# Kernel tuning notes

Hardware: AMD Instinct MI355X
Metric: run time of the kernel (lower is better)

## Reference

```python
import jax, jax.numpy as jnp
import numpy as np

B, D, S, F, C, H, OUT = 4, 60, 512, 158, 64, 128, 1
LN_EPS = 1e-5


def setup_inputs() -> dict:
    key = jax.random.key(0)
    ks = jax.random.split(key, 12)
    g = lambda k, shape, s=0.05: jax.random.normal(k, shape, dtype=jnp.float32) * s
    return dict(
        x=jax.random.normal(ks[0], (B, D, S, F), dtype=jnp.float32),
        feature_mask=jax.random.randint(ks[1], (B, D, S), 0, 2).astype(bool),
        wq=g(ks[2], (F, C)), bq=jnp.zeros((C,), jnp.float32),
        wk=g(ks[3], (F, C)), bk=jnp.zeros((C,), jnp.float32),
        wv=g(ks[4], (F, C)), bv=jnp.zeros((C,), jnp.float32),
        ln_g=jnp.ones((F + C,), jnp.float32), ln_b=jnp.zeros((F + C,), jnp.float32),
        w_ih=g(ks[5], (3 * H, F + C)), w_hh=g(ks[6], (3 * H, H)),
        b_ih=jnp.zeros((3 * H,), jnp.float32), b_hh=jnp.zeros((3 * H,), jnp.float32),
        w1=g(ks[7], (H, H // 2)), b1=jnp.zeros((H // 2,), jnp.float32),
        w2=g(ks[8], (H // 2, OUT)), b2=jnp.zeros((OUT,), jnp.float32),
    )


def reference(x, feature_mask, wq, bq, wk, bk, wv, bv, ln_g, ln_b,
              w_ih, w_hh, b_ih, b_hh, w1, b1, w2, b2):
    b, d, s, f = x.shape
    c = wq.shape[1]
    h_dim = w_hh.shape[1]

    # --- market context attention, vectorized over (batch, days) ---
    Q = x @ wq + bq            # (B,D,S,C)
    K = x @ wk + bk
    V = x @ wv + bv
    scores = jnp.einsum('bdsc,bdtc->bdst', Q, K) / jnp.sqrt(jnp.float32(c))
    scores = jnp.where(feature_mask[:, :, None, :], scores, -1e9)  # mask keys
    attn = jax.nn.softmax(scores, axis=-1)
    ctx = jnp.einsum('bdst,bdtc->bdsc', attn, V)       # (B,D,S,C)
    ctx = jnp.where(feature_mask[..., None], ctx, 0.0)  # mask queries
    denom = jnp.maximum(feature_mask.sum(axis=2), 1).astype(x.dtype)  # (B,D)
    market = ctx.sum(axis=2) / denom[..., None]         # (B,D,C)

    # --- concat + layernorm ---
    aug = jnp.concatenate(
        [x, jnp.broadcast_to(market[:, :, None, :], (b, d, s, c))], axis=-1)
    mu = aug.mean(-1, keepdims=True)
    var = aug.var(-1, keepdims=True)
    aug = (aug - mu) / jnp.sqrt(var + LN_EPS) * ln_g + ln_b  # (B,D,S,F+C)

    # --- GRU over days, batch = B*S independent sequences ---
    seq = aug.transpose(1, 0, 2, 3).reshape(d, b * s, f + c)  # (D, N, F+C)
    x_proj = seq @ w_ih.T + b_ih                               # (D, N, 3H)

    def step(h, xp):
        hp = h @ w_hh.T + b_hh
        xr, xz, xn = jnp.split(xp, 3, axis=-1)
        hr, hz, hn = jnp.split(hp, 3, axis=-1)
        r = jax.nn.sigmoid(xr + hr)
        z = jax.nn.sigmoid(xz + hz)
        n = jnp.tanh(xn + r * hn)
        return (1.0 - z) * n + z * h, None

    h0 = jnp.zeros((b * s, h_dim), x.dtype)
    h_last, _ = jax.lax.scan(step, h0, x_proj)  # last-step output
    h_last = h_last.reshape(b, s, h_dim)

    # --- output head (dropout inactive in eval) ---
    hid = jax.nn.relu(h_last @ w1 + b1)
    return hid @ w2 + b2  # (B, S, OUT)
```

## Files before the change

kernel.cpp:

```cpp
#include <hip/hip_runtime.h>
#include <hip/hip_bf16.h>
#include <math.h>

#define BB 4
#define DD 60
#define SS 512
#define FF 158
#define CC 64
#define HH 128
#define FC 222
#define G3 384
#define NN 2048
#define BDN 240

#define L2E  1.44269504f
#define L2E2 2.88539008f
#define QSCALE 0.18033688f

typedef _Float16 f16x8 __attribute__((ext_vector_type(8)));
typedef float f32x4 __attribute__((ext_vector_type(4)));

__device__ __forceinline__ float exp2_hw(float x){ return __builtin_amdgcn_exp2f(x); }
__device__ __forceinline__ float rcp_hw(float x){ return __builtin_amdgcn_rcpf(x); }

__global__ void prep_kernel(const float* __restrict__ w_ih,
                            const float* __restrict__ wq, const float* __restrict__ wk,
                            const float* __restrict__ w_hh,
                            _Float16* __restrict__ wf16, _Float16* __restrict__ wqk,
                            _Float16* __restrict__ whh16){
    int idx = blockIdx.x*256 + threadIdx.x;
    if (idx < 384*224){
        int n = idx / 224, k = idx % 224;
        float sc = (n < 256) ? L2E : L2E2;
        wf16[idx] = (k < FC) ? (_Float16)(w_ih[n*FC + k] * sc) : (_Float16)0.0f;
    } else if (idx < 384*224 + 128*160){
        int i2 = idx - 384*224;
        int n = i2 / 160, k = i2 % 160;
        float v = 0.0f;
        if (k < FF)
            v = (n < 64) ? wq[k*CC + n] : wk[k*CC + (n-64)];
        wqk[i2] = (_Float16)v;
    } else {
        int i3 = idx - (384*224 + 128*160);
        if (i3 < 384*128){
            int n = i3 / 128;
            float sc = (n < 256) ? L2E : L2E2;
            whh16[i3] = (_Float16)(w_hh[i3] * sc);
        }
    }
}

__global__ __launch_bounds__(256) void qk_kernel(const float* __restrict__ x,
                           const _Float16* __restrict__ wqk,
                           const float* __restrict__ bq, const float* __restrict__ bk,
                           _Float16* __restrict__ Qh, _Float16* __restrict__ Kh){
    __shared__ _Float16 xa[5][64][40];
    int tid  = threadIdx.x;
    int lane = tid & 63, wv = tid >> 6;
    int col  = lane & 15, quad = lane >> 4;
    int row0 = blockIdx.x * 64;

    f16x8 bfr[2][5];
    #pragma unroll
    for (int nt = 0; nt < 2; ++nt){
        int n = wv*32 + nt*16 + col;
        #pragma unroll
        for (int kq = 0; kq < 5; ++kq)
            bfr[nt][kq] = *(const f16x8*)&wqk[n*160 + kq*32 + quad*8];
    }

    if (tid < 128){
        int r = tid >> 1;
        xa[4][r][30 + (tid & 1)] = (_Float16)0.0f;
    }
    {
        const float4* xb4 = (const float4*)(x + (size_t)row0*FF);
        #pragma unroll
        for (int j = 0; j < 10; ++j){
            int i = tid + j*256;
            if (i < 2528){
                float4 v = xb4[i];
                int base = i*4;
                #pragma unroll
                for (int e = 0; e < 4; ++e){
                    int idx = base + e;
                    int r = idx / 158;
                    int k = idx - r*158;
                    xa[k >> 5][r][k & 31] = (_Float16)((&v.x)[e]);
                }
            }
        }
    }
    __syncthreads();

    float bias[2];
    #pragma unroll
    for (int nt = 0; nt < 2; ++nt){
        int n = wv*32 + nt*16 + col;
        bias[nt] = (n < 64) ? bq[n] : bk[n-64];
    }

    #pragma unroll 1
    for (int mt = 0; mt < 4; ++mt){
        f16x8 a[5];
        #pragma unroll
        for (int kq = 0; kq < 5; ++kq)
            a[kq] = *(const f16x8*)&xa[kq][mt*16 + col][quad*8];
        #pragma unroll
        for (int nt = 0; nt < 2; ++nt){
            f32x4 c = {0.0f, 0.0f, 0.0f, 0.0f};
            #pragma unroll
            for (int kq = 0; kq < 5; ++kq)
                c = __builtin_amdgcn_mfma_f32_16x16x32_f16(a[kq], bfr[nt][kq], c, 0, 0, 0);
            int n = wv*32 + nt*16 + col;
            #pragma unroll
            for (int reg = 0; reg < 4; ++reg){
                int row = row0 + mt*16 + quad*4 + reg;
                float val = c[reg] + bias[nt];
                if (n < 64) Qh[(size_t)row*CC + n]      = (_Float16)(val * QSCALE);
                else        Kh[(size_t)row*CC + (n-64)] = (_Float16)val;
            }
        }
    }
}

__global__ __launch_bounds__(512) void attn_kernel(const _Float16* __restrict__ Qh,
                                                   const _Float16* __restrict__ Kh,
                                                   const int* __restrict__ mask,
                                                   const float* __restrict__ x,
                                                   const float* __restrict__ wv,
                                                   const float* __restrict__ bv,
                                                   float* __restrict__ market){
    __shared__ _Float16 kf[2][512][32];
    __shared__ float w_sh[512];
    __shared__ float mk_lds[512];

    int tid  = threadIdx.x;
    int bd   = blockIdx.x;
    int lane = tid & 63, wvw = tid >> 6;
    int col  = lane & 15, quad = lane >> 4;

    const _Float16* qb = Qh + (size_t)(bd*SS)*CC;
    const _Float16* kb = Kh + (size_t)(bd*SS)*CC;

    {
        int t = tid;
        w_sh[t] = 0.0f;
        mk_lds[t] = (mask[bd*SS + t] != 0) ? 1.0f : 0.0f;
    }
    for (int i = tid; i < 4096; i += 512){
        int t = i >> 3, ch = i & 7;
        *(f16x8*)&kf[ch >> 2][t][(ch & 3)*8] = *(const f16x8*)&kb[t*CC + ch*8];
    }

    f16x8 a0[4], a1[4];
    #pragma unroll
    for (int af = 0; af < 4; ++af){
        int row = wvw*64 + af*16 + col;
        a0[af] = *(const f16x8*)&qb[row*CC + quad*8];
        a1[af] = *(const f16x8*)&qb[row*CC + 32 + quad*8];
    }
    __syncthreads();

    float lacc[4][4] = {{0,0,0,0},{0,0,0,0},{0,0,0,0},{0,0,0,0}};
    #pragma unroll 2
    for (int kt = 0; kt < 32; ++kt){
        f16x8 b0 = *(const f16x8*)&kf[0][kt*16 + col][quad*8];
        f16x8 b1 = *(const f16x8*)&kf[1][kt*16 + col][quad*8];
        float mkv = mk_lds[kt*16 + col];
        #pragma unroll
        for (int af = 0; af < 4; ++af){
            f32x4 c = {0.0f, 0.0f, 0.0f, 0.0f};
            c = __builtin_amdgcn_mfma_f32_16x16x32_f16(a0[af], b0, c, 0, 0, 0);
            c = __builtin_amdgcn_mfma_f32_16x16x32_f16(a1[af], b1, c, 0, 0, 0);
            #pragma unroll
            for (int reg = 0; reg < 4; ++reg)
                lacc[af][reg] += exp2_hw(c[reg]) * mkv;
        }
    }
    float crv[4][4];
    #pragma unroll
    for (int af = 0; af < 4; ++af){
        #pragma unroll
        for (int reg = 0; reg < 4; ++reg){
            float l = lacc[af][reg];
            l += __shfl_xor(l, 1, 64);
            l += __shfl_xor(l, 2, 64);
            l += __shfl_xor(l, 4, 64);
            l += __shfl_xor(l, 8, 64);
            int row = wvw*64 + af*16 + quad*4 + reg;
            crv[af][reg] = mk_lds[row] * rcp_hw(l);
        }
    }

    #pragma unroll 2
    for (int kt = 0; kt < 32; ++kt){
        f16x8 b0 = *(const f16x8*)&kf[0][kt*16 + col][quad*8];
        f16x8 b1 = *(const f16x8*)&kf[1][kt*16 + col][quad*8];
        float s = 0.0f;
        #pragma unroll
        for (int af = 0; af < 4; ++af){
            f32x4 c = {0.0f, 0.0f, 0.0f, 0.0f};
            c = __builtin_amdgcn_mfma_f32_16x16x32_f16(a0[af], b0, c, 0, 0, 0);
            c = __builtin_amdgcn_mfma_f32_16x16x32_f16(a1[af], b1, c, 0, 0, 0);
            #pragma unroll
            for (int reg = 0; reg < 4; ++reg)
                s = fmaf(exp2_hw(c[reg]), crv[af][reg], s);
        }
        s += __shfl_xor(s, 16, 64);
        s += __shfl_xor(s, 32, 64);
        if (quad == 0)
            atomicAdd(&w_sh[kt*16 + col], s);
    }
    __syncthreads();

    w_sh[tid] *= mk_lds[tid];
    __syncthreads();

    float* part = (float*)kf;
    {
        int tg = tid >> 8;
        int kk = tid & 255;
        float acc = 0.0f;
        if (kk < FF){
            const float* xb = x + ((size_t)bd*SS + tg*256)*FF + kk;
            #pragma unroll 8
            for (int t = 0; t < 256; ++t)
                acc = fmaf(w_sh[tg*256 + t], xb[(size_t)t*FF], acc);
        }
        part[tg*256 + kk] = acc;
    }
    __syncthreads();
    if (tid < 64){
        int c = tid;
        float m = 0.0f;
        for (int k = 0; k < FF; ++k){
            float y = part[k] + part[256 + k];
            m = fmaf(y, wv[k*CC + c], m);
        }
        float cnt = 0.0f, sw = 0.0f;
        #pragma unroll
        for (int j = 0; j < 8; ++j){
            cnt += mk_lds[c + 64*j];
            sw  += w_sh[c + 64*j];
        }
        #pragma unroll
        for (int o = 1; o < 64; o <<= 1){
            cnt += __shfl_xor(cnt, o, 64);
            sw  += __shfl_xor(sw,  o, 64);
        }
        market[bd*CC + c] = (m + sw*bv[c]) * rcp_hw(fmaxf(cnt, 1.0f));
    }
}

__global__ __launch_bounds__(512, 2) void xproj_kernel(const float* __restrict__ x,
                             const float* __restrict__ market,
                             const float* __restrict__ ln_g, const float* __restrict__ ln_b,
                             const _Float16* __restrict__ wf16, const float* __restrict__ b_ih,
                             _Float16* __restrict__ XP){
    __shared__ _Float16 aug[7][64][32];
    int tid  = threadIdx.x;
    int lane = tid & 63, wv = tid >> 6;
    int col  = lane & 15, quad = lane >> 4;
    int row0 = blockIdx.x * 64;

    f16x8 bfr[3][7];
    #pragma unroll
    for (int nt = 0; nt < 3; ++nt){
        int n = wv*48 + nt*16 + col;
        #pragma unroll
        for (int kq = 0; kq < 7; ++kq)
            bfr[nt][kq] = *(const f16x8*)&wf16[n*224 + kq*32 + quad*8];
    }

    {
        int wrow = wv*8 + (lane >> 3);
        int g    = lane & 7;
        int row  = row0 + wrow;
        int d = row / NN, n = row % NN;
        int b = n >> 9, s = n & 511;
        const float* xr = &x[((size_t)((b*DD + d)*SS) + s)*FF];
        const float* mr = &market[(b*DD + d)*CC];
        float v[28];
        float sum = 0.0f, sq = 0.0f;
        #pragma unroll
        for (int j = 0; j < 28; ++j){
            int f = g + 8*j;
            float vv = 0.0f;
            if (f < FF) vv = xr[f];
            else if (f < FC) vv = mr[f - FF];
            v[j] = vv;
            sum += vv; sq += vv*vv;
        }
        sum += __shfl_xor(sum,1,64); sq += __shfl_xor(sq,1,64);
        sum += __shfl_xor(sum,2,64); sq += __shfl_xor(sq,2,64);
        sum += __shfl_xor(sum,4,64); sq += __shfl_xor(sq,4,64);
        float mu   = sum * (1.0f/222.0f);
        float var  = sq * (1.0f/222.0f) - mu*mu;
        float rstd = rsqrtf(var + 1e-5f);
        #pragma unroll
        for (int j = 0; j < 28; ++j){
            int f = g + 8*j;
            float val = (f < FC) ? ((v[j]-mu)*rstd*ln_g[f] + ln_b[f]) : 0.0f;
            aug[f>>5][wrow][f&31] = (_Float16)val;
        }
    }
    __syncthreads();

    float bias[3];
    #pragma unroll
    for (int nt = 0; nt < 3; ++nt){
        int n = wv*48 + nt*16 + col;
        bias[nt] = b_ih[n] * ((n < 256) ? L2E : L2E2);
    }
    #pragma unroll 1
    for (int mt = 0; mt < 4; ++mt){
        f16x8 a[7];
        #pragma unroll
        for (int kq = 0; kq < 7; ++kq)
            a[kq] = *(const f16x8*)&aug[kq][mt*16 + col][quad*8];
        #pragma unroll
        for (int nt = 0; nt < 3; ++nt){
            f32x4 c = {0.0f, 0.0f, 0.0f, 0.0f};
            #pragma unroll
            for (int kq = 0; kq < 7; ++kq)
                c = __builtin_amdgcn_mfma_f32_16x16x32_f16(a[kq], bfr[nt][kq], c, 0, 0, 0);
            int nn = wv*48 + nt*16 + col;
            #pragma unroll
            for (int reg = 0; reg < 4; ++reg){
                int m = quad*4 + reg;
                XP[(size_t)(row0 + mt*16 + m)*G3 + nn] = (_Float16)(c[reg] + bias[nt]);
            }
        }
    }
}

#define XLOAD(dst, base_) do{                                                   \
    _Pragma("unroll") for (int hf_ = 0; hf_ < 2; ++hf_)                         \
    _Pragma("unroll") for (int rg_ = 0; rg_ < 4; ++rg_)                         \
    _Pragma("unroll") for (int g_ = 0; g_ < 3; ++g_)                            \
        dst[hf_][rg_][g_] = (base_)[rg_*G3 + g_*HH + hf_*16];                   \
}while(0)

#define BARRIER_NODRAIN() asm volatile("s_waitcnt lgkmcnt(0)\ns_barrier" ::: "memory")

#define GRU_STEP(PRD, PWR, XC, XPF, DOPF) do{                                   \
    if (DOPF) { XLOAD(XPF, xp_d + 2*DSTR); }                                    \
    f16x8 a_[4];                                                                \
    _Pragma("unroll") for (int kq = 0; kq < 4; ++kq)                            \
        a_[kq] = *(const f16x8*)&hfrag[PRD][kq][col][quad*8];                   \
    f32x4 c_[3][2];                                                             \
    _Pragma("unroll") for (int g = 0; g < 3; ++g)                               \
    _Pragma("unroll") for (int hf = 0; hf < 2; ++hf){                           \
        f32x4 acc = {0.0f, 0.0f, 0.0f, 0.0f};                                   \
        _Pragma("unroll") for (int kq = 0; kq < 4; ++kq)                        \
            acc = __builtin_amdgcn_mfma_f32_16x16x32_f16(a_[kq], bfr[g][hf][kq], acc, 0,0,0); \
        c_[g][hf] = acc;                                                        \
    }                                                                           \
    _Pragma("unroll") for (int hf = 0; hf < 2; ++hf)                            \
    _Pragma("unroll") for (int rg = 0; rg < 4; ++rg){                           \
        float r_ = rcp_hw(1.0f + exp2_hw(-((float)XC[hf][rg][0] + c_[0][hf][rg] + bh[0][hf]))); \
        float z_ = rcp_hw(1.0f + exp2_hw(-((float)XC[hf][rg][1] + c_[1][hf][rg] + bh[1][hf]))); \
        float e_ = exp2_hw((float)XC[hf][rg][2] + r_*(c_[2][hf][rg] + bh[2][hf])); \
        float n_ = 1.0f - 2.0f*rcp_hw(e_ + 1.0f);                               \
        float h_ = n_ + z_*(hcur[hf][rg] - n_);                                 \
        hcur[hf][rg] = h_;                                                      \
        hfrag[PWR][w][quad*4 + rg][hf*16 + col] = (_Float16)h_;                 \
    }                                                                           \
    xp_d += DSTR;                                                               \
    BARRIER_NODRAIN();                                                          \
}while(0)

__global__ __launch_bounds__(256, 1) void gru_kernel(const _Float16* __restrict__ XP,
                                                     const _Float16* __restrict__ whh16,
                                                     const float* __restrict__ b_hh,
                                                     const float* __restrict__ w1, const float* __restrict__ b1,
                                                     const float* __restrict__ w2, const float* __restrict__ b2,
                                                     float* __restrict__ out){
    __shared__ _Float16 hfrag[2][4][16][40];
    __shared__ float h_sh[16][132];

    const int tid  = threadIdx.x;
    const int lane = tid & 63, w = tid >> 6;
    const int col  = lane & 15, quad = lane >> 4;
    const int row0 = blockIdx.x * 16;

    for (int i = tid; i < 2*4*16*40; i += 256)
        ((_Float16*)hfrag)[i] = (_Float16)0.0f;

    f16x8 bfr[3][2][4];
    #pragma unroll
    for (int g = 0; g < 3; ++g)
    #pragma unroll
    for (int hf = 0; hf < 2; ++hf){
        int n = g*HH + w*32 + hf*16 + col;
        #pragma unroll
        for (int kq = 0; kq < 4; ++kq)
            bfr[g][hf][kq] = *(const f16x8*)&whh16[(size_t)n*HH + kq*32 + quad*8];
    }

    float bh[3][2];
    #pragma unroll
    for (int g = 0; g < 3; ++g)
    #pragma unroll
    for (int hf = 0; hf < 2; ++hf)
        bh[g][hf] = b_hh[g*HH + w*32 + hf*16 + col] * ((g < 2) ? L2E : L2E2);

    const size_t DSTR = (size_t)NN * G3;
    const _Float16* xp_d = XP + (size_t)(row0 + quad*4)*G3 + (w*32 + col);

    _Float16 xA[2][4][3], xB[2][4][3], xC[2][4][3];
    XLOAD(xA, xp_d);
    XLOAD(xB, xp_d + DSTR);

    float hcur[2][4] = {{0,0,0,0},{0,0,0,0}};
    __syncthreads();

    #pragma unroll 1
    for (int ch = 0; ch < 10; ++ch){
        const int pf = (ch < 9);
        GRU_STEP(0, 1, xA, xC, 1);
        GRU_STEP(1, 0, xB, xA, 1);
        GRU_STEP(0, 1, xC, xB, 1);
        GRU_STEP(1, 0, xA, xC, 1);
        GRU_STEP(0, 1, xB, xA, pf);
        GRU_STEP(1, 0, xC, xB, pf);
    }

    #pragma unroll
    for (int hf = 0; hf < 2; ++hf)
    #pragma unroll
    for (int rg = 0; rg < 4; ++rg)
        h_sh[quad*4 + rg][w*32 + hf*16 + col] = hcur[hf][rg];
    __syncthreads();

    {
        int c2 = tid & 63;
        int rb = tid >> 6;
        #pragma unroll
        for (int rr = 0; rr < 4; ++rr){
            int r = rb*4 + rr;
            float acc = 0.0f;
            #pragma unroll 8
            for (int k = 0; k < 128; ++k)
                acc = fmaf(h_sh[r][k], w1[k*64 + c2], acc);
            float hid = fmaxf(acc + b1[c2], 0.0f);
            float o = hid * w2[c2];
            #pragma unroll
            for (int off = 1; off < 64; off <<= 1) o += __shfl_xor(o, off, 64);
            if (c2 == 0) out[row0 + r] = o + b2[0];
        }
    }
}

extern "C" void kernel_launch(void* const* d_in, const int* in_sizes, int n_in,
                              void* d_out, int out_size, void* d_ws, size_t ws_size,
                              hipStream_t stream) {
    const float* x    = (const float*)d_in[0];
    const int*   mask = (const int*)d_in[1];
    const float* wq   = (const float*)d_in[2];
    const float* bq   = (const float*)d_in[3];
    const float* wk   = (const float*)d_in[4];
    const float* bk   = (const float*)d_in[5];
    const float* wv   = (const float*)d_in[6];
    const float* bv   = (const float*)d_in[7];
    const float* ln_g = (const float*)d_in[8];
    const float* ln_b = (const float*)d_in[9];
    const float* w_ih = (const float*)d_in[10];
    const float* w_hh = (const float*)d_in[11];
    const float* b_ih = (const float*)d_in[12];
    const float* b_hh = (const float*)d_in[13];
    const float* w1   = (const float*)d_in[14];
    const float* b1   = (const float*)d_in[15];
    const float* w2   = (const float*)d_in[16];
    const float* b2   = (const float*)d_in[17];

    float* ws = (float*)d_ws;
    _Float16* Qh  = (_Float16*)ws;
    _Float16* Kh  = (_Float16*)(ws + 3932160);
    _Float16* XP  = (_Float16*)ws;
    float* market = ws + 23592960;
    _Float16* wf16 = (_Float16*)(ws + 23608320);
    _Float16* wqk  = (_Float16*)(ws + 23651328);
    _Float16* whh16= (_Float16*)(ws + 23666688);

    prep_kernel<<<648, 256, 0, stream>>>(w_ih, wq, wk, w_hh, wf16, wqk, whh16);
    qk_kernel<<<1920, 256, 0, stream>>>(x, wqk, bq, bk, Qh, Kh);
    attn_kernel<<<240, 512, 0, stream>>>(Qh, Kh, mask, x, wv, bv, market);
    xproj_kernel<<<1920, 512, 0, stream>>>(x, market, ln_g, ln_b, wf16, b_ih, XP);
    gru_kernel<<<128, 256, 0, stream>>>(XP, whh16, b_hh, w1, b1, w2, b2, (float*)d_out);
}
```

Measured before the change: 346.8 us.

## Store GRU input projections in MFMA-fragment layout for vectorized loads

The xproj kernel now writes XP in a packed per-16-row-block layout where each gate column holds 4 consecutive row values contiguously. Each thread then issues one 8-byte store instead of four scattered 2-byte stores. The GRU kernel reads its per-step inputs with six f16x4 loads instead of 24 scalar half loads, which shortens the load path on the serial recurrence. The risk is less coalesced write patterns in xproj and more complex indexing.

```diff
diff --git a/kernel.cpp b/kernel.cpp
--- a/kernel.cpp
+++ b/kernel.cpp
@@ -18,6 +18,7 @@
 #define QSCALE 0.18033688f
 
 typedef _Float16 f16x8 __attribute__((ext_vector_type(8)));
+typedef _Float16 f16x4 __attribute__((ext_vector_type(4)));
 typedef float f32x4 __attribute__((ext_vector_type(4)));
 
 __device__ __forceinline__ float exp2_hw(float x){ return __builtin_amdgcn_exp2f(x); }
@@ -257,7 +258,7 @@
                              const float* __restrict__ market,
                              const float* __restrict__ ln_g, const float* __restrict__ ln_b,
                              const _Float16* __restrict__ wf16, const float* __restrict__ b_ih,
-                             _Float16* __restrict__ XP){
+                             _Float16* __restrict__ XPP){
     __shared__ _Float16 aug[7][64][32];
     int tid  = threadIdx.x;
     int lane = tid & 63, wv = tid >> 6;
@@ -313,12 +314,15 @@
         int n = wv*48 + nt*16 + col;
         bias[nt] = b_ih[n] * ((n < 256) ? L2E : L2E2);
     }
+    const int d    = row0 / NN;
+    const int blk0 = (row0 % NN) >> 4;
     #pragma unroll 1
     for (int mt = 0; mt < 4; ++mt){
         f16x8 a[7];
         #pragma unroll
         for (int kq = 0; kq < 7; ++kq)
             a[kq] = *(const f16x8*)&aug[kq][mt*16 + col][quad*8];
+        _Float16* obase = XPP + ((size_t)(d*128 + blk0 + mt)*G3) * 16 + quad*4;
         #pragma unroll
         for (int nt = 0; nt < 3; ++nt){
             f32x4 c = {0.0f, 0.0f, 0.0f, 0.0f};
@@ -326,20 +330,23 @@
             for (int kq = 0; kq < 7; ++kq)
                 c = __builtin_amdgcn_mfma_f32_16x16x32_f16(a[kq], bfr[nt][kq], c, 0, 0, 0);
             int nn = wv*48 + nt*16 + col;
-            #pragma unroll
-            for (int reg = 0; reg < 4; ++reg){
-                int m = quad*4 + reg;
-                XP[(size_t)(row0 + mt*16 + m)*G3 + nn] = (_Float16)(c[reg] + bias[nt]);
-            }
+            f16x4 pk;
+            pk[0] = (_Float16)(c[0] + bias[nt]);
+            pk[1] = (_Float16)(c[1] + bias[nt]);
+            pk[2] = (_Float16)(c[2] + bias[nt]);
+            pk[3] = (_Float16)(c[3] + bias[nt]);
+            *(f16x4*)(obase + (size_t)nn*16) = pk;
         }
     }
 }
 
 #define XLOAD(dst, base_) do{                                                   \
-    _Pragma("unroll") for (int hf_ = 0; hf_ < 2; ++hf_)                         \
-    _Pragma("unroll") for (int rg_ = 0; rg_ < 4; ++rg_)                         \
-    _Pragma("unroll") for (int g_ = 0; g_ < 3; ++g_)                            \
-        dst[hf_][rg_][g_] = (base_)[rg_*G3 + g_*HH + hf_*16];                   \
+    dst[0][0] = *(const f16x4*)((base_));                                       \
+    dst[0][1] = *(const f16x4*)((base_) + 128*16);                              \
+    dst[0][2] = *(const f16x4*)((base_) + 256*16);                              \
+    dst[1][0] = *(const f16x4*)((base_) + 16*16);                               \
+    dst[1][1] = *(const f16x4*)((base_) + 144*16);                              \
+    dst[1][2] = *(const f16x4*)((base_) + 272*16);                              \
 }while(0)
 
 #define BARRIER_NODRAIN() asm volatile("s_waitcnt lgkmcnt(0)\ns_barrier" ::: "memory")
@@ -359,9 +366,9 @@
     }                                                                           \
     _Pragma("unroll") for (int hf = 0; hf < 2; ++hf)                            \
     _Pragma("unroll") for (int rg = 0; rg < 4; ++rg){                           \
-        float r_ = rcp_hw(1.0f + exp2_hw(-((float)XC[hf][rg][0] + c_[0][hf][rg] + bh[0][hf]))); \
-        float z_ = rcp_hw(1.0f + exp2_hw(-((float)XC[hf][rg][1] + c_[1][hf][rg] + bh[1][hf]))); \
-        float e_ = exp2_hw((float)XC[hf][rg][2] + r_*(c_[2][hf][rg] + bh[2][hf])); \
+        float r_ = rcp_hw(1.0f + exp2_hw(-((float)XC[hf][0][rg] + c_[0][hf][rg] + bh[0][hf]))); \
+        float z_ = rcp_hw(1.0f + exp2_hw(-((float)XC[hf][1][rg] + c_[1][hf][rg] + bh[1][hf]))); \
+        float e_ = exp2_hw((float)XC[hf][2][rg] + r_*(c_[2][hf][rg] + bh[2][hf])); \
         float n_ = 1.0f - 2.0f*rcp_hw(e_ + 1.0f);                               \
         float h_ = n_ + z_*(hcur[hf][rg] - n_);                                 \
         hcur[hf][rg] = h_;                                                      \
@@ -371,7 +378,7 @@
     BARRIER_NODRAIN();                                                          \
 }while(0)
 
-__global__ __launch_bounds__(256, 1) void gru_kernel(const _Float16* __restrict__ XP,
+__global__ __launch_bounds__(256, 1) void gru_kernel(const _Float16* __restrict__ XPP,
                                                      const _Float16* __restrict__ whh16,
                                                      const float* __restrict__ b_hh,
                                                      const float* __restrict__ w1, const float* __restrict__ b1,
@@ -406,10 +413,10 @@
     for (int hf = 0; hf < 2; ++hf)
         bh[g][hf] = b_hh[g*HH + w*32 + hf*16 + col] * ((g < 2) ? L2E : L2E2);
 
-    const size_t DSTR = (size_t)NN * G3;
-    const _Float16* xp_d = XP + (size_t)(row0 + quad*4)*G3 + (w*32 + col);
-
-    _Float16 xA[2][4][3], xB[2][4][3], xC[2][4][3];
+    const size_t DSTR = (size_t)128 * G3 * 16;
+    const _Float16* xp_d = XPP + ((size_t)blockIdx.x*G3 + (w*32 + col))*16 + quad*4;
+
+    f16x4 xA[2][3], xB[2][3], xC[2][3];
     XLOAD(xA, xp_d);
     XLOAD(xB, xp_d + DSTR);
 
@@ -478,7 +485,7 @@
     float* ws = (float*)d_ws;
     _Float16* Qh  = (_Float16*)ws;
     _Float16* Kh  = (_Float16*)(ws + 3932160);
-    _Float16* XP  = (_Float16*)ws;
+    _Float16* XPP = (_Float16*)ws;
     float* market = ws + 23592960;
     _Float16* wf16 = (_Float16*)(ws + 23608320);
     _Float16* wqk  = (_Float16*)(ws + 23651328);
@@ -487,6 +494,6 @@
     prep_kernel<<<648, 256, 0, stream>>>(w_ih, wq, wk, w_hh, wf16, wqk, whh16);
     qk_kernel<<<1920, 256, 0, stream>>>(x, wqk, bq, bk, Qh, Kh);
     attn_kernel<<<240, 512, 0, stream>>>(Qh, Kh, mask, x, wv, bv, market);
-    xproj_kernel<<<1920, 512, 0, stream>>>(x, market, ln_g, ln_b, wf16, b_ih, XP);
-    gru_kernel<<<128, 256, 0, stream>>>(XP, whh16, b_hh, w1, b1, w2, b2, (float*)d_out);
-}
+    xproj_kernel<<<1920, 512, 0, stream>>>(x, market, ln_g, ln_b, wf16, b_ih, XPP);
+    gru_kernel<<<128, 256, 0, stream>>>(XPP, whh16, b_hh, w1, b1, w2, b2, (float*)d_out);
+}
```

New measurement: 343.4 us. No clear change (-1.0%).
